# Kernel optimization log

Hardware: AMD Instinct MI355X
Metric: run time of the kernel (lower is better)

## Reference

```python
import jax, jax.numpy as jnp
import numpy as np

V, DW, DH, OUT = 50000, 300, 50, 4
B, T = 1024, 200


def setup_inputs() -> dict:
    key = jax.random.key(0)
    ks = jax.random.split(key, 9)
    x = jax.random.randint(ks[0], (B, T), 0, V)
    lengs = jax.random.randint(ks[1], (B,), 1, T + 1)  # valid lengths >= 1
    k = 1.0 / np.sqrt(DH)
    emb = jax.random.normal(ks[2], (V, DW), jnp.float32)
    emb = emb.at[0].set(0.0)  # padding_idx=0
    w_ih = jax.random.uniform(ks[3], (4 * DH, DW), jnp.float32, -k, k)
    w_hh = jax.random.uniform(ks[4], (4 * DH, DH), jnp.float32, -k, k)
    b_ih = jax.random.uniform(ks[5], (4 * DH,), jnp.float32, -k, k)
    b_hh = jax.random.uniform(ks[6], (4 * DH,), jnp.float32, -k, k)
    w_out = jax.random.uniform(ks[7], (OUT, DH), jnp.float32, -k, k)
    b_out = jax.random.uniform(ks[8], (OUT,), jnp.float32, -k, k)
    return {"x": x, "lengs": lengs, "emb": emb, "w_ih": w_ih, "w_hh": w_hh,
            "b_ih": b_ih, "b_hh": b_hh, "w_out": w_out, "b_out": b_out}


def reference(x, lengs, emb, w_ih, w_hh, b_ih, b_hh, w_out, b_out):
    b, t = x.shape
    xe = emb[x]                                        # [B,T,DW]
    mask = jnp.arange(t)[None, :] < lengs[:, None]     # [B,T] valid steps
    bias = b_ih + b_hh                                 # [4*DH]

    def step(carry, inp):
        h, c = carry
        x_t, m_t = inp                                 # [B,DW], [B]
        g = x_t @ w_ih.T + h @ w_hh.T + bias           # [B,4*DH]
        i, f, gg, o = jnp.split(g, 4, axis=-1)         # torch gate order i,f,g,o
        c_new = jax.nn.sigmoid(f) * c + jax.nn.sigmoid(i) * jnp.tanh(gg)
        h_new = jax.nn.sigmoid(o) * jnp.tanh(c_new)
        m = m_t[:, None]
        # packed-sequence semantics: state frozen past each sequence's length
        return (jnp.where(m, h_new, h), jnp.where(m, c_new, c)), None

    h0 = jnp.zeros((b, DH), xe.dtype)
    (h, _), _ = jax.lax.scan(step, (h0, h0),
                             (xe.transpose(1, 0, 2), mask.T))
    logits = h @ w_out.T + b_out                       # hidden.view(B,-1) -> Linear
    return jax.nn.softmax(logits, axis=1)
```

## Files before the change

kernel.cpp:

```cpp
#include <hip/hip_runtime.h>
#include <math.h>

#define VOCAB 50000
#define DW 300
#define DH 50
#define G4 200
#define BATCH 1024
#define TMAX 200
#define OUTC 4

__global__ __launch_bounds__(256) void transpose_wih(
    const float* __restrict__ w_ih, float* __restrict__ w_T)
{
    int i = blockIdx.x * 256 + threadIdx.x;
    if (i < G4 * DW) {
        int u = i / DW, k = i % DW;
        int u2 = (u % DH) * 4 + (u / DH);
        w_T[k * G4 + u2] = w_ih[i];
    }
}

__global__ __launch_bounds__(256, 2) void proj_kernel(
    const float* __restrict__ emb, const float* __restrict__ w_T,
    const float* __restrict__ b_ih, const float* __restrict__ b_hh,
    float* __restrict__ emb_proj)
{
    __shared__ __align__(16) float e_s[100 * 108];
    const int tid = threadIdx.x;
    const int v0 = blockIdx.x * 100;
    const int m_idx = tid / 25;
    const int n_idx = tid % 25;

    float acc[10][8];
#pragma unroll
    for (int m = 0; m < 10; m++)
#pragma unroll
        for (int c = 0; c < 8; c++) acc[m][c] = 0.f;

    const float* wcol = w_T + n_idx * 8;

    for (int kc = 0; kc < DW; kc += 100) {
        __syncthreads();
        for (int i = tid; i < 2500; i += 256) {
            int r = i / 25, c = i % 25;
            float4 v = *(const float4*)&emb[(size_t)(v0 + r) * DW + kc + c * 4];
            *(float4*)&e_s[r * 108 + c * 4] = v;
        }
        __syncthreads();

        if (tid < 250) {
            float4 wa[4], wb[4];
#pragma unroll
            for (int j = 0; j < 4; j++) {
                const float* p = wcol + (size_t)(kc + j) * G4;
                wa[j] = *(const float4*)p;
                wb[j] = *(const float4*)(p + 4);
            }
            for (int kk = 0; kk < 25; kk++) {
                float4 na[4], nb[4];
                int kn = kc + ((kk < 24) ? (kk + 1) : kk) * 4;
#pragma unroll
                for (int j = 0; j < 4; j++) {
                    const float* p = wcol + (size_t)(kn + j) * G4;
                    na[j] = *(const float4*)p;
                    nb[j] = *(const float4*)(p + 4);
                }
                float4 e4[10];
#pragma unroll
                for (int m = 0; m < 10; m++)
                    e4[m] = *(const float4*)&e_s[(m_idx * 10 + m) * 108 + kk * 4];
#pragma unroll
                for (int j = 0; j < 4; j++) {
#pragma unroll
                    for (int m = 0; m < 10; m++) {
                        float ev = (j == 0) ? e4[m].x : (j == 1) ? e4[m].y
                                 : (j == 2) ? e4[m].z : e4[m].w;
                        acc[m][0] = fmaf(ev, wa[j].x, acc[m][0]);
                        acc[m][1] = fmaf(ev, wa[j].y, acc[m][1]);
                        acc[m][2] = fmaf(ev, wa[j].z, acc[m][2]);
                        acc[m][3] = fmaf(ev, wa[j].w, acc[m][3]);
                        acc[m][4] = fmaf(ev, wb[j].x, acc[m][4]);
                        acc[m][5] = fmaf(ev, wb[j].y, acc[m][5]);
                        acc[m][6] = fmaf(ev, wb[j].z, acc[m][6]);
                        acc[m][7] = fmaf(ev, wb[j].w, acc[m][7]);
                    }
                }
#pragma unroll
                for (int j = 0; j < 4; j++) { wa[j] = na[j]; wb[j] = nb[j]; }
            }
        }
    }

    if (tid < 250) {
        float bias[8];
#pragma unroll
        for (int c = 0; c < 8; c++) {
            int u2 = n_idx * 8 + c;
            int u  = (u2 & 3) * DH + (u2 >> 2);
            bias[c] = b_ih[u] + b_hh[u];
        }
#pragma unroll
        for (int m = 0; m < 10; m++) {
            float* dst = &emb_proj[(size_t)(v0 + m_idx * 10 + m) * G4 + n_idx * 8];
            *(float4*)dst = make_float4(acc[m][0] + bias[0], acc[m][1] + bias[1],
                                        acc[m][2] + bias[2], acc[m][3] + bias[3]);
            *(float4*)(dst + 4) = make_float4(acc[m][4] + bias[4], acc[m][5] + bias[5],
                                              acc[m][6] + bias[6], acc[m][7] + bias[7]);
        }
    }
}

__device__ __forceinline__ float dpp_xor1(float x) {
    return __int_as_float(__builtin_amdgcn_update_dpp(
        0, __float_as_int(x), 0xB1, 0xF, 0xF, true));
}

__global__ __launch_bounds__(128, 2) void lstm_kernel(
    const int* __restrict__ x, const int* __restrict__ lengs,
    const float* __restrict__ emb_proj, const float* __restrict__ w_hh,
    const float* __restrict__ w_out, const float* __restrict__ b_out,
    float* __restrict__ out)
{
    __shared__ __align__(16) float hbuf[2][52];
    __shared__ int x_s[TMAX];
    __shared__ float red[OUTC];

    const int tid = threadIdx.x;
    const int b   = blockIdx.x;
    const int u   = tid >> 1;
    const int uu  = (u < DH) ? u : 0;
    const int odd = tid & 1;
    const int len = lengs[b];

    for (int i = tid; i < TMAX; i += 128) x_s[i] = x[b * TMAX + i];
    if (tid < 52) hbuf[0][tid] = 0.f;

    float wA[DH], wB[DH];
    {
        const float* rA = w_hh + (size_t)((2 * odd) * DH + uu) * DH;
        const float* rB = w_hh + (size_t)((2 * odd + 1) * DH + uu) * DH;
#pragma unroll
        for (int k = 0; k < 25; k++) {
            float2 a  = *(const float2*)(rA + 2 * k);
            float2 bb = *(const float2*)(rB + 2 * k);
            wA[2 * k] = a.x;  wA[2 * k + 1] = a.y;
            wB[2 * k] = bb.x; wB[2 * k + 1] = bb.y;
        }
    }
#pragma unroll
    for (int k = 0; k < DH; k++) {
        asm volatile("" : "+v"(wA[k]));
        asm volatile("" : "+v"(wB[k]));
    }
    __syncthreads();

    const int col = (u < DH) ? (tid * 2) : 0;
    const float* ep = emb_proj;
    float2 p0 = *(const float2*)(ep + (size_t)x_s[0] * G4 + col);
    float2 p1 = *(const float2*)(ep + (size_t)x_s[1] * G4 + col);
    float2 p2 = *(const float2*)(ep + (size_t)x_s[2] * G4 + col);
    float c_reg = 0.f;

    for (int t = 0; t < len; t++) {
        float2 cur = p0; p0 = p1; p1 = p2;
        int nt = t + 3; nt = (nt < TMAX) ? nt : TMAX - 1;
        p2 = *(const float2*)(ep + (size_t)x_s[nt] * G4 + col);

        const float* hb = hbuf[t & 1];
        float accA0 = 0.f, accA1 = 0.f, accB0 = 0.f, accB1 = 0.f;
#pragma unroll
        for (int k4 = 0; k4 < 12; k4++) {
            float4 h4 = *(const float4*)(hb + 4 * k4);
            if ((k4 & 1) == 0) {
                accA0 = fmaf(h4.x, wA[4*k4], fmaf(h4.y, wA[4*k4+1],
                        fmaf(h4.z, wA[4*k4+2], fmaf(h4.w, wA[4*k4+3], accA0))));
                accB0 = fmaf(h4.x, wB[4*k4], fmaf(h4.y, wB[4*k4+1],
                        fmaf(h4.z, wB[4*k4+2], fmaf(h4.w, wB[4*k4+3], accB0))));
            } else {
                accA1 = fmaf(h4.x, wA[4*k4], fmaf(h4.y, wA[4*k4+1],
                        fmaf(h4.z, wA[4*k4+2], fmaf(h4.w, wA[4*k4+3], accA1))));
                accB1 = fmaf(h4.x, wB[4*k4], fmaf(h4.y, wB[4*k4+1],
                        fmaf(h4.z, wB[4*k4+2], fmaf(h4.w, wB[4*k4+3], accB1))));
            }
        }
        {
            float2 h2 = *(const float2*)(hb + 48);
            accA0 = fmaf(h2.x, wA[48], fmaf(h2.y, wA[49], accA0));
            accB1 = fmaf(h2.x, wB[48], fmaf(h2.y, wB[49], accB1));
        }
        float gA = cur.x + accA0 + accA1;
        float gB = cur.y + accB0 + accB1;

        float yA = odd ? 2.f * gA : gA;
        float sA = 1.f / (1.f + __expf(-yA));
        float vA = odd ? fmaf(2.f, sA, -1.f) : sA;
        float vB = 1.f / (1.f + __expf(-gB));

        float oA = dpp_xor1(vA);
        float oB = dpp_xor1(vB);
        float si = odd ? oA : vA;
        float sf = odd ? oB : vB;
        float tg = odd ? vA : oA;
        float so = odd ? vB : oB;

        float cn = fmaf(sf, c_reg, si * tg);
        c_reg = cn;
        float th = fmaf(2.f, 1.f / (1.f + __expf(-2.f * cn)), -1.f);
        float hn = so * th;
        if (!odd && u < DH) hbuf[(t + 1) & 1][u] = hn;
        __syncthreads();
    }

    const float* hf = hbuf[len & 1];
    if (tid < OUTC) {
        float lg = b_out[tid];
        const float* wo = w_out + tid * DH;
#pragma unroll
        for (int k = 0; k < DH; k++) lg = fmaf(hf[k], wo[k], lg);
        red[tid] = lg;
    }
    if (tid < OUTC) {
        float m = fmaxf(fmaxf(red[0], red[1]), fmaxf(red[2], red[3]));
        float s = 0.f;
#pragma unroll
        for (int j = 0; j < OUTC; j++) s += __expf(red[j] - m);
        out[b * OUTC + tid] = __expf(red[tid] - m) / s;
    }
}

extern "C" void kernel_launch(void* const* d_in, const int* in_sizes, int n_in,
                              void* d_out, int out_size, void* d_ws, size_t ws_size,
                              hipStream_t stream) {
    const int*   x     = (const int*)d_in[0];
    const int*   lengs = (const int*)d_in[1];
    const float* emb   = (const float*)d_in[2];
    const float* w_ih  = (const float*)d_in[3];
    const float* w_hh  = (const float*)d_in[4];
    const float* b_ih  = (const float*)d_in[5];
    const float* b_hh  = (const float*)d_in[6];
    const float* w_out = (const float*)d_in[7];
    const float* b_out = (const float*)d_in[8];
    float* out = (float*)d_out;

    float* emb_proj = (float*)d_ws;
    float* w_T      = emb_proj + (size_t)VOCAB * G4;

    hipLaunchKernelGGL(transpose_wih, dim3((G4 * DW + 255) / 256), dim3(256),
                       0, stream, w_ih, w_T);
    hipLaunchKernelGGL(proj_kernel, dim3(VOCAB / 100), dim3(256), 0, stream,
                       emb, w_T, b_ih, b_hh, emb_proj);
    hipLaunchKernelGGL(lstm_kernel, dim3(BATCH), dim3(128), 0, stream,
                       x, lengs, emb_proj, w_hh, w_out, b_out, out);
}
```

Before: 307.1 us.

## Split LSTM recurrence to one thread per gate row with quad DPP broadcast

The recurrent kernel moves from 128 threads, each computing two gate rows, to 256 threads, each computing one gate row of the hidden-to-hidden product. Gates are exchanged inside each group of four lanes via DPP quad broadcasts. This halves the serial FMA chain per thread and the weight registers held per thread, cutting per-step latency on the sequential critical path. In exchange it doubles the thread count per block, which may reduce occupancy, and adds barrier cost with four waves per block.

```diff
diff --git a/kernel.cpp b/kernel.cpp
--- a/kernel.cpp
+++ b/kernel.cpp
@@ -110,12 +110,13 @@
     }
 }
 
-__device__ __forceinline__ float dpp_xor1(float x) {
+template <int CTRL>
+__device__ __forceinline__ float qbcast(float x) {
     return __int_as_float(__builtin_amdgcn_update_dpp(
-        0, __float_as_int(x), 0xB1, 0xF, 0xF, true));
-}
-
-__global__ __launch_bounds__(128, 2) void lstm_kernel(
+        0, __float_as_int(x), CTRL, 0xF, 0xF, true));
+}
+
+__global__ __launch_bounds__(256, 2) void lstm_kernel(
     const int* __restrict__ x, const int* __restrict__ lengs,
     const float* __restrict__ emb_proj, const float* __restrict__ w_hh,
     const float* __restrict__ w_out, const float* __restrict__ b_out,
@@ -125,89 +126,81 @@
     __shared__ int x_s[TMAX];
     __shared__ float red[OUTC];
 
-    const int tid = threadIdx.x;
-    const int b   = blockIdx.x;
-    const int u   = tid >> 1;
-    const int uu  = (u < DH) ? u : 0;
-    const int odd = tid & 1;
-    const int len = lengs[b];
-
-    for (int i = tid; i < TMAX; i += 128) x_s[i] = x[b * TMAX + i];
+    const int tid  = threadIdx.x;
+    const int b    = blockIdx.x;
+    const int gate = tid & 3;
+    const int unit = tid >> 2;
+    const int uu   = (unit < DH) ? unit : DH - 1;
+    const int col  = (tid < G4) ? tid : 0;
+    const int len  = lengs[b];
+
+    for (int i = tid; i < TMAX; i += 256) x_s[i] = x[b * TMAX + i];
     if (tid < 52) hbuf[0][tid] = 0.f;
 
-    float wA[DH], wB[DH];
-    {
-        const float* rA = w_hh + (size_t)((2 * odd) * DH + uu) * DH;
-        const float* rB = w_hh + (size_t)((2 * odd + 1) * DH + uu) * DH;
-#pragma unroll
-        for (int k = 0; k < 25; k++) {
-            float2 a  = *(const float2*)(rA + 2 * k);
-            float2 bb = *(const float2*)(rB + 2 * k);
-            wA[2 * k] = a.x;  wA[2 * k + 1] = a.y;
-            wB[2 * k] = bb.x; wB[2 * k + 1] = bb.y;
-        }
-    }
-#pragma unroll
-    for (int k = 0; k < DH; k++) {
-        asm volatile("" : "+v"(wA[k]));
-        asm volatile("" : "+v"(wB[k]));
-    }
+    const float* wr = w_hh + (size_t)(gate * DH + uu) * DH;
+#define LDW(J) ({ float2 ta_ = *(const float2*)(wr + 4 * (J));                \
+                  float2 tb_ = *(const float2*)(wr + 4 * (J) + 2);            \
+                  make_float4(ta_.x, ta_.y, tb_.x, tb_.y); })
+    const float4 W0 = LDW(0),  W1 = LDW(1),  W2  = LDW(2),  W3  = LDW(3);
+    const float4 W4 = LDW(4),  W5 = LDW(5),  W6  = LDW(6),  W7  = LDW(7);
+    const float4 W8 = LDW(8),  W9 = LDW(9),  W10 = LDW(10), W11 = LDW(11);
+    const float2 W12 = *(const float2*)(wr + 48);
+#undef LDW
+
     __syncthreads();
 
-    const int col = (u < DH) ? (tid * 2) : 0;
     const float* ep = emb_proj;
-    float2 p0 = *(const float2*)(ep + (size_t)x_s[0] * G4 + col);
-    float2 p1 = *(const float2*)(ep + (size_t)x_s[1] * G4 + col);
-    float2 p2 = *(const float2*)(ep + (size_t)x_s[2] * G4 + col);
+    float p0 = ep[(size_t)x_s[0] * G4 + col];
+    float p1 = ep[(size_t)x_s[1] * G4 + col];
+    float p2 = ep[(size_t)x_s[2] * G4 + col];
     float c_reg = 0.f;
 
     for (int t = 0; t < len; t++) {
-        float2 cur = p0; p0 = p1; p1 = p2;
+        float cur = p0; p0 = p1; p1 = p2;
         int nt = t + 3; nt = (nt < TMAX) ? nt : TMAX - 1;
-        p2 = *(const float2*)(ep + (size_t)x_s[nt] * G4 + col);
+        p2 = ep[(size_t)x_s[nt] * G4 + col];
 
         const float* hb = hbuf[t & 1];
-        float accA0 = 0.f, accA1 = 0.f, accB0 = 0.f, accB1 = 0.f;
-#pragma unroll
-        for (int k4 = 0; k4 < 12; k4++) {
-            float4 h4 = *(const float4*)(hb + 4 * k4);
-            if ((k4 & 1) == 0) {
-                accA0 = fmaf(h4.x, wA[4*k4], fmaf(h4.y, wA[4*k4+1],
-                        fmaf(h4.z, wA[4*k4+2], fmaf(h4.w, wA[4*k4+3], accA0))));
-                accB0 = fmaf(h4.x, wB[4*k4], fmaf(h4.y, wB[4*k4+1],
-                        fmaf(h4.z, wB[4*k4+2], fmaf(h4.w, wB[4*k4+3], accB0))));
-            } else {
-                accA1 = fmaf(h4.x, wA[4*k4], fmaf(h4.y, wA[4*k4+1],
-                        fmaf(h4.z, wA[4*k4+2], fmaf(h4.w, wA[4*k4+3], accA1))));
-                accB1 = fmaf(h4.x, wB[4*k4], fmaf(h4.y, wB[4*k4+1],
-                        fmaf(h4.z, wB[4*k4+2], fmaf(h4.w, wB[4*k4+3], accB1))));
-            }
-        }
-        {
-            float2 h2 = *(const float2*)(hb + 48);
-            accA0 = fmaf(h2.x, wA[48], fmaf(h2.y, wA[49], accA0));
-            accB1 = fmaf(h2.x, wB[48], fmaf(h2.y, wB[49], accB1));
-        }
-        float gA = cur.x + accA0 + accA1;
-        float gB = cur.y + accB0 + accB1;
-
-        float yA = odd ? 2.f * gA : gA;
-        float sA = 1.f / (1.f + __expf(-yA));
-        float vA = odd ? fmaf(2.f, sA, -1.f) : sA;
-        float vB = 1.f / (1.f + __expf(-gB));
-
-        float oA = dpp_xor1(vA);
-        float oB = dpp_xor1(vB);
-        float si = odd ? oA : vA;
-        float sf = odd ? oB : vB;
-        float tg = odd ? vA : oA;
-        float so = odd ? vB : oB;
-
-        float cn = fmaf(sf, c_reg, si * tg);
+        float4 h0  = *(const float4*)(hb + 0);
+        float4 h1  = *(const float4*)(hb + 4);
+        float4 h2  = *(const float4*)(hb + 8);
+        float4 h3  = *(const float4*)(hb + 12);
+        float4 h4  = *(const float4*)(hb + 16);
+        float4 h5  = *(const float4*)(hb + 20);
+        float4 h6  = *(const float4*)(hb + 24);
+        float4 h7  = *(const float4*)(hb + 28);
+        float4 h8  = *(const float4*)(hb + 32);
+        float4 h9  = *(const float4*)(hb + 36);
+        float4 h10 = *(const float4*)(hb + 40);
+        float4 h11 = *(const float4*)(hb + 44);
+        float2 h12 = *(const float2*)(hb + 48);
+
+#define DOT4(A, H, W)                                                         \
+        A = fmaf((H).x, (W).x, fmaf((H).y, (W).y,                             \
+            fmaf((H).z, (W).z, fmaf((H).w, (W).w, A))));
+        float a0 = cur, a1 = 0.f, a2 = 0.f, a3 = 0.f;
+        DOT4(a0, h0, W0)  DOT4(a1, h1, W1)  DOT4(a2, h2,  W2)  DOT4(a3, h3,  W3)
+        DOT4(a0, h4, W4)  DOT4(a1, h5, W5)  DOT4(a2, h6,  W6)  DOT4(a3, h7,  W7)
+        DOT4(a0, h8, W8)  DOT4(a1, h9, W9)  DOT4(a2, h10, W10) DOT4(a3, h11, W11)
+        a1 = fmaf(h12.x, W12.x, fmaf(h12.y, W12.y, a1));
+#undef DOT4
+        float g = (a0 + a1) + (a2 + a3);
+
+        const bool isg = (gate == 2);
+        float arg = isg ? (-2.f * g) : (-g);
+        float r   = 1.f / (1.f + __expf(arg));
+        float v   = isg ? fmaf(2.f, r, -1.f) : r;
+
+        float si = qbcast<0x00>(v);
+        float sf = qbcast<0x55>(v);
+        float tc = qbcast<0xAA>(v);
+        float so = qbcast<0xFF>(v);
+
+        float cn = fmaf(sf, c_reg, si * tc);
         c_reg = cn;
         float th = fmaf(2.f, 1.f / (1.f + __expf(-2.f * cn)), -1.f);
         float hn = so * th;
-        if (!odd && u < DH) hbuf[(t + 1) & 1][u] = hn;
+        if ((gate == 0) && (tid < G4)) hbuf[(t + 1) & 1][unit] = hn;
         __syncthreads();
     }
 
@@ -249,6 +242,6 @@
                        0, stream, w_ih, w_T);
     hipLaunchKernelGGL(proj_kernel, dim3(VOCAB / 100), dim3(256), 0, stream,
                        emb, w_T, b_ih, b_hh, emb_proj);
-    hipLaunchKernelGGL(lstm_kernel, dim3(BATCH), dim3(128), 0, stream,
+    hipLaunchKernelGGL(lstm_kernel, dim3(BATCH), dim3(256), 0, stream,
                        x, lengs, emb_proj, w_hh, w_out, b_out, out);
 }
```

New measurement: 347.5 us. 13.2% more time.
